# Kernel optimization log

Hardware: AMD Instinct MI355X
Metric: run time of the kernel (lower is better)

The kernel has to match this reference:

```python
import jax, jax.numpy as jnp
import numpy as np

# static config (matches init_kwargs)
T_K = 3      # Time_kernel
K = 3        # spatial_kernel_side_length
C = 64       # dim_hidden
H = 4        # num_head
D = 16       # dim_head
NL = 2       # num_layers
F = 3        # dim_feature
N, S1, S2 = 32, 32, 32
P = K // 2
L1 = T_K // 2
M = T_K * K * K
EPS = 1e-5


def _neighbor_mask():
    # spatial_neighbor_mask with an all-ones city mask: offset (k1,k2) is a valid
    # neighbor of cell (s1,s2) iff it lands inside the grid.
    m = np.zeros((S1, S2, K, K), dtype=bool)
    s1 = np.arange(S1); s2 = np.arange(S2)
    for k1 in range(K):
        v1 = (s1 + k1 - P >= 0) & (s1 + k1 - P < S1)
        for k2 in range(K):
            v2 = (s2 + k2 - P >= 0) & (s2 + k2 - P < S2)
            m[:, :, k1, k2] = v1[:, None] & v2[None, :]
    mf = m.reshape(S1, S2, K * K)
    # tiled across Time_kernel, flattened in (t, k1, k2) order like the torch code
    return np.tile(mf[:, :, None, :], (1, 1, T_K, 1)).reshape(S1, S2, M)

_MASK = jnp.asarray(_neighbor_mask())


def _forward(x, W_in, b_in, W_out, b_out, Wq, bq, Wk, bk, Wv, bv):
    # BatchNorm2d (training-mode batch stats, affine = identity init)
    mean = x.mean(axis=(0, 1, 2))
    var = ((x - mean) ** 2).mean(axis=(0, 1, 2))
    h = (x - mean) * jax.lax.rsqrt(var + EPS)
    h = h @ W_in + b_in  # [N,S1,S2,C]

    for l in range(NL):
        res = h  # res_block_thickness = 1 -> residual every layer
        q = (h @ Wq[l] + bq[l]).reshape(N, S1, S2, H, D)
        # spatial unfold (nn.Unfold, padding=K//2, stride=1)
        hp = jnp.pad(h, ((0, 0), (P, P), (P, P), (0, 0)))
        u = jnp.stack([jnp.stack([hp[:, k1:k1 + S1, k2:k2 + S2, :]
                                  for k2 in range(K)]) for k1 in range(K)])  # [K,K,N,S1,S2,C]
        # time unfold (zero-padded shifts along N)
        up = jnp.pad(u, ((0, 0), (0, 0), (L1, L1), (0, 0), (0, 0), (0, 0)))
        ut = jnp.stack([up[:, :, t:t + N] for t in range(T_K)])  # [T,K,K,N,S1,S2,C]
        # per-offset single-Linear MLPs (kernel_neurons=[C,C]), batched over T,K,K
        ks = jnp.einsum('tijnabc,tijcd->nabtijd', ut, Wk[l]) + bk[l]
        vs = jnp.einsum('tijnabc,tijcd->nabtijd', ut, Wv[l]) + bv[l]
        kM = ks.reshape(N, S1, S2, M, H, D)
        vM = vs.reshape(N, S1, S2, M, H, D)
        # unscaled dot-product attention over valid neighbors (masked == dropped)
        sc = jnp.einsum('nabmhd,nabhd->nabhm', kM, q)
        sc = jnp.where(_MASK[None, :, :, None, :], sc, -1e30)
        w = jax.nn.softmax(sc, axis=-1)
        h = jnp.einsum('nabhm,nabmhd->nabhd', w, vM).reshape(N, S1, S2, C)
        h = h + res

    return h @ W_out + b_out  # [N,S1,S2,F]


def setup_inputs() -> dict:
    key = jax.random.key(0)
    k = jax.random.split(key, 11)
    s = 0.05
    return {
        'x': jax.random.normal(k[0], (N, S1, S2, F), jnp.float32),
        'W_in': jax.random.normal(k[1], (F, C), jnp.float32) * s,
        'b_in': jax.random.normal(k[2], (C,), jnp.float32) * s,
        'W_out': jax.random.normal(k[3], (C, F), jnp.float32) * s,
        'b_out': jax.random.normal(k[4], (F,), jnp.float32) * s,
        'Wq': jax.random.normal(k[5], (NL, C, C), jnp.float32) * s,
        'bq': jax.random.normal(k[6], (NL, C), jnp.float32) * s,
        'Wk': jax.random.normal(k[7], (NL, T_K, K, K, C, C), jnp.float32) * s,
        'bk': jax.random.normal(k[8], (NL, T_K, K, K, C), jnp.float32) * s,
        'Wv': jax.random.normal(k[9], (NL, T_K, K, K, C, C), jnp.float32) * s,
        'bv': jax.random.normal(k[10], (NL, T_K, K, K, C), jnp.float32) * s,
    }


def reference(x, W_in, b_in, W_out, b_out, Wq, bq, Wk, bk, Wv, bv):
    return _forward(x, W_in, b_in, W_out, b_out, Wq, bq, Wk, bk, Wv, bv)
```

## Files before the change

kernel.cpp:

```cpp
#include <hip/hip_runtime.h>
#include <hip/hip_bf16.h>


typedef short short8_t __attribute__((ext_vector_type(8)));
typedef float floatx4 __attribute__((ext_vector_type(4)));

__device__ __forceinline__ short f2bs(float f) {
    __hip_bfloat16 h = __float2bfloat16(f);
    return *reinterpret_cast<short*>(&h);
}
__device__ __forceinline__ float bs2f(short s) {
    union { unsigned u; float f; } v;
    v.u = ((unsigned)(unsigned short)s) << 16;
    return v.f;
}
__device__ __forceinline__ int hn_idx(int rowid, int chunk) {
    return rowid * 64 + ((chunk ^ (rowid & 7)) << 3);
}

__global__ void prep_kernel(const float* __restrict__ Wq, const float* __restrict__ Wk,
                            const float* __restrict__ Wv, short* __restrict__ dst,
                            const float* __restrict__ x, float* __restrict__ sums) {
    if (blockIdx.x < 220) {
        int t = blockIdx.x * 256 + threadIdx.x;
        if (t >= 110 * 512) return;
        int mat  = t >> 9;
        int rem  = t & 511;
        int kk   = rem >> 8;
        int nt   = (rem >> 6) & 3;
        int lane = rem & 63;
        int krow = kk * 32 + (lane >> 4) * 8;
        int col  = nt * 16 + (lane & 15);
        const float* W;
        if (mat < 2)       W = Wq + mat * 4096;
        else if (mat < 56) W = Wk + (mat - 2) * 4096;
        else               W = Wv + (mat - 56) * 4096;
        short8_t v;
        #pragma unroll
        for (int j = 0; j < 8; ++j) v[j] = f2bs(W[(krow + j) * 64 + col]);
        *(short8_t*)&dst[(size_t)mat * 4096 + ((kk * 4 + nt) * 64 + lane) * 8] = v;
    } else {
        int bid = blockIdx.x - 220;
        int t = bid * 256 + threadIdx.x;
        const float4* x4 = (const float4*)x;
        float4 v0 = x4[t * 3 + 0], v1 = x4[t * 3 + 1], v2 = x4[t * 3 + 2];
        float vv[6];
        vv[0] = v0.x + v0.w + v1.z + v2.y;
        vv[1] = v0.y + v1.x + v1.w + v2.z;
        vv[2] = v0.z + v1.y + v2.x + v2.w;
        vv[3] = v0.x*v0.x + v0.w*v0.w + v1.z*v1.z + v2.y*v2.y;
        vv[4] = v0.y*v0.y + v1.x*v1.x + v1.w*v1.w + v2.z*v2.z;
        vv[5] = v0.z*v0.z + v1.y*v1.y + v2.x*v2.x + v2.w*v2.w;
        #pragma unroll
        for (int i = 0; i < 6; ++i) {
            #pragma unroll
            for (int off = 1; off < 64; off <<= 1) vv[i] += __shfl_xor(vv[i], off);
        }
        __shared__ float part[4][6];
        if ((threadIdx.x & 63) == 0) {
            #pragma unroll
            for (int i = 0; i < 6; ++i) part[threadIdx.x >> 6][i] = vv[i];
        }
        __syncthreads();
        if (threadIdx.x < 6)
            sums[bid * 8 + threadIdx.x] = part[0][threadIdx.x] + part[1][threadIdx.x] +
                                          part[2][threadIdx.x] + part[3][threadIdx.x];
    }
}

template <bool FIRST>
__global__ __launch_bounds__(512, 4)
void layer_fused(const float* __restrict__ x, const float* __restrict__ sums,
                 const float* __restrict__ W_in, const float* __restrict__ b_in,
                 const short* __restrict__ hbf_in, short* __restrict__ hbf_out,
                 const float* __restrict__ Wout, const float* __restrict__ bout,
                 float* __restrict__ out,
                 const short* __restrict__ wqB, const float* __restrict__ bq,
                 const short* __restrict__ wkB, const float* __restrict__ bk,
                 const short* __restrict__ wvB, const float* __restrict__ bv) {
    __shared__ short HnS[324 * 64];
    __shared__ float Waux[256];
    __shared__ float bn6[6];

    const int tid = threadIdx.x;
    const int bb0 = blockIdx.x * 4, a = blockIdx.y, nb = blockIdx.z;

    if (FIRST) {
        if (tid < 3) {
            float s = 0.f, qq = 0.f;
            #pragma unroll
            for (int p = 0; p < 32; ++p) { s += sums[p * 8 + tid]; qq += sums[p * 8 + 3 + tid]; }
            float mean = s * (1.f / 32768.f);
            float var  = qq * (1.f / 32768.f) - mean * mean;
            bn6[tid]     = mean;
            bn6[3 + tid] = rsqrtf(var + 1e-5f);
        }
        if (tid < 192)      Waux[tid] = W_in[tid];
        else if (tid < 256) Waux[tid] = b_in[tid - 192];
    } else {
        if (tid < 192)      Waux[tid] = Wout[tid];
        else if (tid < 195) Waux[tid] = bout[tid - 192];
    }
    __syncthreads();

    float mean0 = 0, mean1 = 0, mean2 = 0, rs0 = 0, rs1 = 0, rs2 = 0;
    if (FIRST) {
        mean0 = bn6[0]; mean1 = bn6[1]; mean2 = bn6[2];
        rs0 = bn6[3]; rs1 = bn6[4]; rs2 = bn6[5];
    }

    for (int id = tid; id < 2592; id += 512) {
        int rowid = id >> 3, cc = id & 7;
        int r = rowid % 18;
        int rw = rowid / 18;
        int spa = rw / 6, jcol = rw - spa * 6;
        int aa = a + spa - 1, bb = bb0 + jcol - 1;
        int n  = nb * 16 + r - 1;
        short8_t v = {0, 0, 0, 0, 0, 0, 0, 0};
        if ((unsigned)n < 32u && (unsigned)aa < 32u && (unsigned)bb < 32u) {
            int cell = (n * 32 + aa) * 32 + bb;
            if (FIRST) {
                float xn0 = (x[cell*3+0] - mean0) * rs0;
                float xn1 = (x[cell*3+1] - mean1) * rs1;
                float xn2 = (x[cell*3+2] - mean2) * rs2;
                #pragma unroll
                for (int j = 0; j < 8; ++j) {
                    int c = cc * 8 + j;
                    float h = Waux[192+c] + xn0*Waux[c] + xn1*Waux[64+c] + xn2*Waux[128+c];
                    v[j] = f2bs(h);
                }
            } else {
                v = *(const short8_t*)&hbf_in[cell * 64 + cc * 8];
            }
        }
        *(short8_t*)&HnS[hn_idx(rowid, cc)] = v;
    }
    __syncthreads();

    const int lane = tid & 63;
    const int wv8  = tid >> 6;
    const int w    = wv8 & 3;
    const int g2   = wv8 >> 2;
    const int e    = lane & 15;
    const int q    = lane >> 4;
    const int c0   = w * 16 + q * 4;

    bool va[3], vb[6];
    #pragma unroll
    for (int d = 0; d < 3; ++d) va[d] = (unsigned)(a + d - 1) < 32u;
    #pragma unroll
    for (int j = 0; j < 6; ++j) vb[j] = (unsigned)(bb0 + j - 1) < 32u;

    floatx4 qv[4];
    {
        short8_t wq0 = *(const short8_t*)&wqB[((0 * 4 + w) * 64 + lane) * 8];
        short8_t wq1 = *(const short8_t*)&wqB[((1 * 4 + w) * 64 + lane) * 8];
        const float4 bq4 = *(const float4*)&bq[c0];
        #pragma unroll
        for (int ci = 0; ci < 4; ++ci) {
            const int row = (6 + ci + 1) * 18 + e + 1;
            short8_t h0 = *(const short8_t*)&HnS[hn_idx(row, q)];
            short8_t h1 = *(const short8_t*)&HnS[hn_idx(row, 4 + q)];
            floatx4 acc = {0, 0, 0, 0};
            acc = __builtin_amdgcn_mfma_f32_16x16x32_bf16(wq0, h0, acc, 0, 0, 0);
            acc = __builtin_amdgcn_mfma_f32_16x16x32_bf16(wq1, h1, acc, 0, 0, 0);
            qv[ci][0] = acc[0] + bq4.x; qv[ci][1] = acc[1] + bq4.y;
            qv[ci][2] = acc[2] + bq4.z; qv[ci][3] = acc[3] + bq4.w;
        }
    }

    floatx4 o[4] = {{0,0,0,0},{0,0,0,0},{0,0,0,0},{0,0,0,0}};
    float ss[4] = {0.f, 0.f, 0.f, 0.f};

    const int mstart = g2 ? 14 : 0;
    const int mend   = g2 ? 27 : 14;
    for (int m = mstart; m < mend; ++m) {
        const int t  = (m * 57) >> 9;
        const int sp = m - 9 * t;
        const int di = (sp * 11) >> 5;
        const int dj = sp - 3 * di;
        if (!va[di]) continue;
        short8_t wk0 = *(const short8_t*)&wkB[m * 4096 + ((0 * 4 + w) * 64 + lane) * 8];
        short8_t wk1 = *(const short8_t*)&wkB[m * 4096 + ((1 * 4 + w) * 64 + lane) * 8];
        short8_t wv0 = *(const short8_t*)&wvB[m * 4096 + ((0 * 4 + w) * 64 + lane) * 8];
        short8_t wv1 = *(const short8_t*)&wvB[m * 4096 + ((1 * 4 + w) * 64 + lane) * 8];
        const float4 bk4 = *(const float4*)&bk[m * 64 + c0];
        const float4 bv4 = *(const float4*)&bv[m * 64 + c0];
        const int rowb = (di * 6 + dj) * 18 + e + t;
        #pragma unroll
        for (int ci = 0; ci < 4; ++ci) {
            if (!vb[dj + ci]) continue;
            const int row = rowb + ci * 18;
            short8_t h0 = *(const short8_t*)&HnS[hn_idx(row, q)];
            short8_t h1 = *(const short8_t*)&HnS[hn_idx(row, 4 + q)];
            floatx4 kacc = {0, 0, 0, 0};
            kacc = __builtin_amdgcn_mfma_f32_16x16x32_bf16(wk0, h0, kacc, 0, 0, 0);
            kacc = __builtin_amdgcn_mfma_f32_16x16x32_bf16(wk1, h1, kacc, 0, 0, 0);
            floatx4 vacc = {0, 0, 0, 0};
            vacc = __builtin_amdgcn_mfma_f32_16x16x32_bf16(wv0, h0, vacc, 0, 0, 0);
            vacc = __builtin_amdgcn_mfma_f32_16x16x32_bf16(wv1, h1, vacc, 0, 0, 0);
            float p = (kacc[0] + bk4.x) * qv[ci][0] + (kacc[1] + bk4.y) * qv[ci][1]
                    + (kacc[2] + bk4.z) * qv[ci][2] + (kacc[3] + bk4.w) * qv[ci][3];
            p += __shfl_xor(p, 16);
            p += __shfl_xor(p, 32);
            float wgt = __expf(p);
            ss[ci] += wgt;
            o[ci][0] += wgt * (vacc[0] + bv4.x);
            o[ci][1] += wgt * (vacc[1] + bv4.y);
            o[ci][2] += wgt * (vacc[2] + bv4.z);
            o[ci][3] += wgt * (vacc[3] + bv4.w);
        }
    }

    __syncthreads();
    float* stbuf = (float*)HnS;
    if (g2 == 1) {
        #pragma unroll
        for (int ci = 0; ci < 4; ++ci) {
            float* d = &stbuf[(((w * 64 + lane) * 4) + ci) * 5];
            d[0] = ss[ci];
            d[1] = o[ci][0]; d[2] = o[ci][1]; d[3] = o[ci][2]; d[4] = o[ci][3];
        }
    }
    __syncthreads();
    if (g2 == 0) {
        #pragma unroll
        for (int ci = 0; ci < 4; ++ci) {
            const float* d = &stbuf[(((w * 64 + lane) * 4) + ci) * 5];
            float inv = 1.0f / (ss[ci] + d[0]);
            o[ci][0] = (o[ci][0] + d[1]) * inv;
            o[ci][1] = (o[ci][1] + d[2]) * inv;
            o[ci][2] = (o[ci][2] + d[3]) * inv;
            o[ci][3] = (o[ci][3] + d[4]) * inv;
        }
    }

    const int n = nb * 16 + e;
    if (FIRST) {
        if (g2 == 0) {
            #pragma unroll
            for (int ci = 0; ci < 4; ++ci) {
                int cell = (n * 32 + a) * 32 + bb0 + ci;
                float xn0 = (x[cell*3+0] - mean0) * rs0;
                float xn1 = (x[cell*3+1] - mean1) * rs1;
                float xn2 = (x[cell*3+2] - mean2) * rs2;
                short4 hb; short* hbp = (short*)&hb;
                #pragma unroll
                for (int i = 0; i < 4; ++i) {
                    int c = c0 + i;
                    float res = Waux[192+c] + xn0*Waux[c] + xn1*Waux[64+c] + xn2*Waux[128+c];
                    hbp[i] = f2bs(o[ci][i] + res);
                }
                *(short4*)&hbf_out[cell * 64 + c0] = hb;
            }
        }
    } else {
        __syncthreads();
        float* hf = (float*)HnS;
        if (g2 == 0) {
            #pragma unroll
            for (int ci = 0; ci < 4; ++ci) {
                int cell = (n * 32 + a) * 32 + bb0 + ci;
                short4 hb = *(const short4*)&hbf_in[cell * 64 + c0];
                float* d = &hf[(ci * 16 + e) * 68 + c0];
                d[0] = o[ci][0] + bs2f(hb.x);
                d[1] = o[ci][1] + bs2f(hb.y);
                d[2] = o[ci][2] + bs2f(hb.z);
                d[3] = o[ci][3] + bs2f(hb.w);
            }
        }
        __syncthreads();
        if (tid < 192) {
            int rowglob = tid / 3, f = tid - rowglob * 3;
            int ci = rowglob >> 4, row = rowglob & 15;
            float acc = Waux[192 + f];
            #pragma unroll 8
            for (int cc = 0; cc < 64; ++cc) acc += hf[rowglob * 68 + cc] * Waux[cc * 3 + f];
            int nn = nb * 16 + row;
            out[((nn * 32 + a) * 32 + bb0 + ci) * 3 + f] = acc;
        }
    }
}

extern "C" void kernel_launch(void* const* d_in, const int* in_sizes, int n_in,
                              void* d_out, int out_size, void* d_ws, size_t ws_size,
                              hipStream_t stream) {
    const float* x     = (const float*)d_in[0];
    const float* W_in  = (const float*)d_in[1];
    const float* b_in  = (const float*)d_in[2];
    const float* W_out = (const float*)d_in[3];
    const float* b_out = (const float*)d_in[4];
    const float* Wq    = (const float*)d_in[5];
    const float* bq    = (const float*)d_in[6];
    const float* Wk    = (const float*)d_in[7];
    const float* bk    = (const float*)d_in[8];
    const float* Wv    = (const float*)d_in[9];
    const float* bv    = (const float*)d_in[10];

    float* ws    = (float*)d_ws;
    float* sums  = ws;
    short* h1bf  = (short*)(ws + 256);
    short* wB    = h1bf + 2097152;
    float* out   = (float*)d_out;

    prep_kernel<<<252, 256, 0, stream>>>(Wq, Wk, Wv, wB, x, sums);

    const short* wq0 = wB;                const short* wq1 = wB + 4096;
    const short* wk0 = wB + 2 * 4096;     const short* wk1 = wB + (2 + 27) * 4096;
    const short* wv0 = wB + 56 * 4096;    const short* wv1 = wB + (56 + 27) * 4096;

    dim3 grid(8, 32, 2);
    layer_fused<true><<<grid, 512, 0, stream>>>(
        x, sums, W_in, b_in, nullptr, h1bf, nullptr, nullptr, nullptr,
        wq0, bq, wk0, bk, wv0, bv);
    layer_fused<false><<<grid, 512, 0, stream>>>(
        nullptr, nullptr, nullptr, nullptr, h1bf, nullptr, W_out, b_out, out,
        wq1, bq + 64, wk1, bk + 1728, wv1, bv + 1728);
}
```

Baseline: 144.3 us.

## Halve per-block column tile, raise occupancy, fold biases into MFMA accumulators, permlane reduction

Each block now covers 2 spatial columns instead of 4, which shrinks the shared halo tile from 324 to 216 rows and doubles the grid to 1024 blocks. Launch bounds are raised to allow 8 blocks per CU. Biases are preloaded into the MFMA accumulators instead of being added afterwards, and the cross-quad dot-product reduction uses v_permlane16/32 swap instructions instead of shuffles. The halo redundancy ratio rises (more reloads of neighbours per output) and the tighter register budget risks spills, in exchange for more parallelism and fewer VALU ops.

```diff
diff --git a/kernel.cpp b/kernel.cpp
--- a/kernel.cpp
+++ b/kernel.cpp
@@ -16,6 +16,14 @@
 }
 __device__ __forceinline__ int hn_idx(int rowid, int chunk) {
     return rowid * 64 + ((chunk ^ (rowid & 7)) << 3);
+}
+__device__ __forceinline__ float quad_sum(float p) {
+    float a = p, b = p;
+    asm("v_permlane16_swap_b32 %0, %1" : "+v"(a), "+v"(b));
+    float s = a + b;
+    float c = s, d = s;
+    asm("v_permlane32_swap_b32 %0, %1" : "+v"(c), "+v"(d));
+    return c + d;
 }
 
 __global__ void prep_kernel(const float* __restrict__ Wq, const float* __restrict__ Wk,
@@ -69,7 +77,7 @@
 }
 
 template <bool FIRST>
-__global__ __launch_bounds__(512, 4)
+__global__ __launch_bounds__(512, 8)
 void layer_fused(const float* __restrict__ x, const float* __restrict__ sums,
                  const float* __restrict__ W_in, const float* __restrict__ b_in,
                  const short* __restrict__ hbf_in, short* __restrict__ hbf_out,
@@ -78,12 +86,12 @@
                  const short* __restrict__ wqB, const float* __restrict__ bq,
                  const short* __restrict__ wkB, const float* __restrict__ bk,
                  const short* __restrict__ wvB, const float* __restrict__ bv) {
-    __shared__ short HnS[324 * 64];
+    __shared__ short HnS[216 * 64];
     __shared__ float Waux[256];
     __shared__ float bn6[6];
 
     const int tid = threadIdx.x;
-    const int bb0 = blockIdx.x * 4, a = blockIdx.y, nb = blockIdx.z;
+    const int bb0 = blockIdx.x * 2, a = blockIdx.y, nb = blockIdx.z;
 
     if (FIRST) {
         if (tid < 3) {
@@ -109,11 +117,11 @@
         rs0 = bn6[3]; rs1 = bn6[4]; rs2 = bn6[5];
     }
 
-    for (int id = tid; id < 2592; id += 512) {
+    for (int id = tid; id < 1728; id += 512) {
         int rowid = id >> 3, cc = id & 7;
         int r = rowid % 18;
         int rw = rowid / 18;
-        int spa = rw / 6, jcol = rw - spa * 6;
+        int spa = rw >> 2, jcol = rw & 3;
         int aa = a + spa - 1, bb = bb0 + jcol - 1;
         int n  = nb * 16 + r - 1;
         short8_t v = {0, 0, 0, 0, 0, 0, 0, 0};
@@ -145,32 +153,31 @@
     const int q    = lane >> 4;
     const int c0   = w * 16 + q * 4;
 
-    bool va[3], vb[6];
+    bool va[3], vb[4];
     #pragma unroll
     for (int d = 0; d < 3; ++d) va[d] = (unsigned)(a + d - 1) < 32u;
     #pragma unroll
-    for (int j = 0; j < 6; ++j) vb[j] = (unsigned)(bb0 + j - 1) < 32u;
-
-    floatx4 qv[4];
+    for (int j = 0; j < 4; ++j) vb[j] = (unsigned)(bb0 + j - 1) < 32u;
+
+    floatx4 qv[2];
     {
         short8_t wq0 = *(const short8_t*)&wqB[((0 * 4 + w) * 64 + lane) * 8];
         short8_t wq1 = *(const short8_t*)&wqB[((1 * 4 + w) * 64 + lane) * 8];
         const float4 bq4 = *(const float4*)&bq[c0];
         #pragma unroll
-        for (int ci = 0; ci < 4; ++ci) {
-            const int row = (6 + ci + 1) * 18 + e + 1;
+        for (int ci = 0; ci < 2; ++ci) {
+            const int row = (5 + ci) * 18 + e + 1;
             short8_t h0 = *(const short8_t*)&HnS[hn_idx(row, q)];
             short8_t h1 = *(const short8_t*)&HnS[hn_idx(row, 4 + q)];
-            floatx4 acc = {0, 0, 0, 0};
+            floatx4 acc = {bq4.x, bq4.y, bq4.z, bq4.w};
             acc = __builtin_amdgcn_mfma_f32_16x16x32_bf16(wq0, h0, acc, 0, 0, 0);
             acc = __builtin_amdgcn_mfma_f32_16x16x32_bf16(wq1, h1, acc, 0, 0, 0);
-            qv[ci][0] = acc[0] + bq4.x; qv[ci][1] = acc[1] + bq4.y;
-            qv[ci][2] = acc[2] + bq4.z; qv[ci][3] = acc[3] + bq4.w;
-        }
-    }
-
-    floatx4 o[4] = {{0,0,0,0},{0,0,0,0},{0,0,0,0},{0,0,0,0}};
-    float ss[4] = {0.f, 0.f, 0.f, 0.f};
+            qv[ci] = acc;
+        }
+    }
+
+    floatx4 o[2] = {{0,0,0,0},{0,0,0,0}};
+    float ss[2] = {0.f, 0.f};
 
     const int mstart = g2 ? 14 : 0;
     const int mend   = g2 ? 27 : 14;
@@ -186,29 +193,28 @@
         short8_t wv1 = *(const short8_t*)&wvB[m * 4096 + ((1 * 4 + w) * 64 + lane) * 8];
         const float4 bk4 = *(const float4*)&bk[m * 64 + c0];
         const float4 bv4 = *(const float4*)&bv[m * 64 + c0];
-        const int rowb = (di * 6 + dj) * 18 + e + t;
-        #pragma unroll
-        for (int ci = 0; ci < 4; ++ci) {
+        const int rowb = (di * 4 + dj) * 18 + e + t;
+        #pragma unroll
+        for (int ci = 0; ci < 2; ++ci) {
             if (!vb[dj + ci]) continue;
             const int row = rowb + ci * 18;
             short8_t h0 = *(const short8_t*)&HnS[hn_idx(row, q)];
             short8_t h1 = *(const short8_t*)&HnS[hn_idx(row, 4 + q)];
-            floatx4 kacc = {0, 0, 0, 0};
+            floatx4 kacc = {bk4.x, bk4.y, bk4.z, bk4.w};
             kacc = __builtin_amdgcn_mfma_f32_16x16x32_bf16(wk0, h0, kacc, 0, 0, 0);
             kacc = __builtin_amdgcn_mfma_f32_16x16x32_bf16(wk1, h1, kacc, 0, 0, 0);
-            floatx4 vacc = {0, 0, 0, 0};
+            floatx4 vacc = {bv4.x, bv4.y, bv4.z, bv4.w};
             vacc = __builtin_amdgcn_mfma_f32_16x16x32_bf16(wv0, h0, vacc, 0, 0, 0);
             vacc = __builtin_amdgcn_mfma_f32_16x16x32_bf16(wv1, h1, vacc, 0, 0, 0);
-            float p = (kacc[0] + bk4.x) * qv[ci][0] + (kacc[1] + bk4.y) * qv[ci][1]
-                    + (kacc[2] + bk4.z) * qv[ci][2] + (kacc[3] + bk4.w) * qv[ci][3];
-            p += __shfl_xor(p, 16);
-            p += __shfl_xor(p, 32);
+            float p = kacc[0] * qv[ci][0] + kacc[1] * qv[ci][1]
+                    + kacc[2] * qv[ci][2] + kacc[3] * qv[ci][3];
+            p = quad_sum(p);
             float wgt = __expf(p);
             ss[ci] += wgt;
-            o[ci][0] += wgt * (vacc[0] + bv4.x);
-            o[ci][1] += wgt * (vacc[1] + bv4.y);
-            o[ci][2] += wgt * (vacc[2] + bv4.z);
-            o[ci][3] += wgt * (vacc[3] + bv4.w);
+            o[ci][0] += wgt * vacc[0];
+            o[ci][1] += wgt * vacc[1];
+            o[ci][2] += wgt * vacc[2];
+            o[ci][3] += wgt * vacc[3];
         }
     }
 
@@ -216,8 +222,8 @@
     float* stbuf = (float*)HnS;
     if (g2 == 1) {
         #pragma unroll
-        for (int ci = 0; ci < 4; ++ci) {
-            float* d = &stbuf[(((w * 64 + lane) * 4) + ci) * 5];
+        for (int ci = 0; ci < 2; ++ci) {
+            float* d = &stbuf[(((w * 64 + lane) * 2) + ci) * 5];
             d[0] = ss[ci];
             d[1] = o[ci][0]; d[2] = o[ci][1]; d[3] = o[ci][2]; d[4] = o[ci][3];
         }
@@ -225,8 +231,8 @@
     __syncthreads();
     if (g2 == 0) {
         #pragma unroll
-        for (int ci = 0; ci < 4; ++ci) {
-            const float* d = &stbuf[(((w * 64 + lane) * 4) + ci) * 5];
+        for (int ci = 0; ci < 2; ++ci) {
+            const float* d = &stbuf[(((w * 64 + lane) * 2) + ci) * 5];
             float inv = 1.0f / (ss[ci] + d[0]);
             o[ci][0] = (o[ci][0] + d[1]) * inv;
             o[ci][1] = (o[ci][1] + d[2]) * inv;
@@ -239,7 +245,7 @@
     if (FIRST) {
         if (g2 == 0) {
             #pragma unroll
-            for (int ci = 0; ci < 4; ++ci) {
+            for (int ci = 0; ci < 2; ++ci) {
                 int cell = (n * 32 + a) * 32 + bb0 + ci;
                 float xn0 = (x[cell*3+0] - mean0) * rs0;
                 float xn1 = (x[cell*3+1] - mean1) * rs1;
@@ -259,10 +265,10 @@
         float* hf = (float*)HnS;
         if (g2 == 0) {
             #pragma unroll
-            for (int ci = 0; ci < 4; ++ci) {
+            for (int ci = 0; ci < 2; ++ci) {
                 int cell = (n * 32 + a) * 32 + bb0 + ci;
                 short4 hb = *(const short4*)&hbf_in[cell * 64 + c0];
-                float* d = &hf[(ci * 16 + e) * 68 + c0];
+                float* d = &hf[(ci * 16 + e) * 65 + c0];
                 d[0] = o[ci][0] + bs2f(hb.x);
                 d[1] = o[ci][1] + bs2f(hb.y);
                 d[2] = o[ci][2] + bs2f(hb.z);
@@ -270,12 +276,12 @@
             }
         }
         __syncthreads();
-        if (tid < 192) {
+        if (tid < 96) {
             int rowglob = tid / 3, f = tid - rowglob * 3;
             int ci = rowglob >> 4, row = rowglob & 15;
             float acc = Waux[192 + f];
             #pragma unroll 8
-            for (int cc = 0; cc < 64; ++cc) acc += hf[rowglob * 68 + cc] * Waux[cc * 3 + f];
+            for (int cc = 0; cc < 64; ++cc) acc += hf[rowglob * 65 + cc] * Waux[cc * 3 + f];
             int nn = nb * 16 + row;
             out[((nn * 32 + a) * 32 + bb0 + ci) * 3 + f] = acc;
         }
@@ -309,7 +315,7 @@
     const short* wk0 = wB + 2 * 4096;     const short* wk1 = wB + (2 + 27) * 4096;
     const short* wv0 = wB + 56 * 4096;    const short* wv1 = wB + (56 + 27) * 4096;
 
-    dim3 grid(8, 32, 2);
+    dim3 grid(16, 32, 2);
     layer_fused<true><<<grid, 512, 0, stream>>>(
         x, sums, W_in, b_in, nullptr, h1bf, nullptr, nullptr, nullptr,
         wq0, bq, wk0, bk, wv0, bv);
```

Result: slower. 291.3 us (+101.9%).
